# Kernel optimization log

Hardware: AMD Instinct MI355X
Metric: run time of the kernel (lower is better)

The kernel has to match this reference:

```python
import jax, jax.numpy as jnp
import numpy as np

NUM_NODES = 50000
NUM_EDGES = 800000
NUM_LABEL_EDGES = 100000
F_IN, F_HID, F_OUT = 128, 128, 64


def gcn_conv(x, src, dst, W, b, n):
    # PyG GCNConv: h = x @ W; add self-loops; symmetric normalization
    # deg counted on destination (col), including self-loop (+1).
    h = x @ W
    deg = jax.ops.segment_sum(jnp.ones(src.shape, h.dtype), dst, num_segments=n) + 1.0
    dinv = jax.lax.rsqrt(deg)  # deg >= 1 always (self-loop)
    norm = dinv[src] * dinv[dst]                       # [E]
    agg = jax.ops.segment_sum(h[src] * norm[:, None], dst, num_segments=n)
    agg = agg + h * (dinv * dinv)[:, None]             # self-loop term dinv[i]^2 * h[i]
    return agg + b


def setup_inputs() -> dict:
    key = jax.random.key(0)
    ks = jax.random.split(key, 9)
    x = jax.random.normal(ks[0], (NUM_NODES, F_IN), dtype=jnp.float32)
    edge_index = jax.random.randint(ks[1], (2, NUM_EDGES), 0, NUM_NODES, dtype=jnp.int64)
    edge_label_index = jax.random.randint(ks[2], (2, NUM_LABEL_EDGES), 0, NUM_NODES, dtype=jnp.int64)
    def glorot(k, fi, fo):
        s = (6.0 / (fi + fo)) ** 0.5
        return jax.random.uniform(k, (fi, fo), jnp.float32, -s, s)
    return {
        "x": x,
        "edge_index": edge_index,
        "edge_label_index": edge_label_index,
        "W1": glorot(ks[3], F_IN, F_HID),  "b1": jnp.zeros((F_HID,), jnp.float32),
        "W2": glorot(ks[4], F_HID, F_HID), "b2": jnp.zeros((F_HID,), jnp.float32),
        "W3": glorot(ks[5], F_HID, F_OUT), "b3": jnp.zeros((F_OUT,), jnp.float32),
    }


def reference(x, edge_index, edge_label_index, W1, b1, W2, b2, W3, b3):
    src, dst = edge_index[0], edge_index[1]
    z = jax.nn.relu(gcn_conv(x, src, dst, W1, b1, NUM_NODES))
    z = jax.nn.relu(gcn_conv(z, src, dst, W2, b2, NUM_NODES))
    z = gcn_conv(z, src, dst, W3, b3, NUM_NODES)
    # decode: dot product of endpoint embeddings per label edge
    return jnp.sum(z[edge_label_index[0]] * z[edge_label_index[1]], axis=-1)
```

## Files before the change

kernel.cpp:

```cpp
#include <hip/hip_runtime.h>
#include <hip/hip_bf16.h>
#include <stdint.h>

#define NN 50000
#define NE 800000
#define NL 100000
#define SLOTS 64
#define PADROW 50000

#define NB 196
#define BSH 8
#define BCAP 5376

typedef __attribute__((ext_vector_type(8))) short bf16x8;
typedef __attribute__((ext_vector_type(4))) float f32x4;
typedef __attribute__((ext_vector_type(4))) unsigned int u32x4;
typedef __attribute__((ext_vector_type(2))) unsigned int u32x2;
typedef __attribute__((ext_vector_type(8))) unsigned short u16x8;

__device__ __forceinline__ float asf(unsigned int u) {
    union { unsigned int i; float f; } c; c.i = u; return c.f;
}
__device__ __forceinline__ float bflo(unsigned int x) { return asf(x << 16); }
__device__ __forceinline__ float bfhi(unsigned int x) { return asf(x & 0xffff0000u); }
__device__ __forceinline__ unsigned short f2bf(float f) {
    union { float f; unsigned int i; } c; c.f = f;
    unsigned int u = c.i + (0x7fffu + ((c.i >> 16) & 1u));
    return (unsigned short)(u >> 16);
}

__device__ __forceinline__ void dma16(const unsigned short* g, char* l) {
    __builtin_amdgcn_global_load_lds(
        (const __attribute__((address_space(1))) unsigned int*)g,
        (__attribute__((address_space(3))) unsigned int*)l, 16, 0, 0);
}

__global__ void k_wprep(const float* __restrict__ W1, const float* __restrict__ W2,
                        const float* __restrict__ W3, unsigned short* __restrict__ Wt,
                        int* __restrict__ cursor, unsigned int* __restrict__ padA,
                        unsigned int* __restrict__ padB) {
    int idx = blockIdx.x * 256 + threadIdx.x;
    if (idx < NB) cursor[idx] = 0;
    if (idx < 64) padA[idx] = 0;
    else if (idx < 128) padB[idx - 64] = 0;
    const float* W; unsigned short* O; int base, Mloc;
    if (idx < 16384)      { W = W1; O = Wt;         base = idx;         Mloc = 128; }
    else if (idx < 32768) { W = W2; O = Wt + 16384; base = idx - 16384; Mloc = 128; }
    else                  { W = W3; O = Wt + 32768; base = idx - 32768; Mloc = 64;  }
    int n = base >> 7, k = base & 127;
    O[base] = f2bf(W[k * Mloc + n]);
}

__global__ __launch_bounds__(256) void k_bin(
        const int* __restrict__ src, const int* __restrict__ dst,
        int* __restrict__ cursor, unsigned int* __restrict__ binbuf) {
    __shared__ int hcnt[NB];
    __shared__ int hbase[NB];
    __shared__ unsigned int epk[2048];
    int tid = threadIdx.x;
    if (tid < NB) hcnt[tid] = 0;
    __syncthreads();
    int e0 = blockIdx.x * 2048;
    int e1 = min(e0 + 2048, NE);
    for (int e = e0 + tid; e < e1; e += 256) {
        int d = dst[e], s = src[e];
        atomicAdd(&hcnt[d >> BSH], 1);
        epk[e - e0] = (unsigned int)s | ((unsigned int)d << 16);
    }
    __syncthreads();
    if (tid < NB) { hbase[tid] = atomicAdd(&cursor[tid], hcnt[tid]); hcnt[tid] = 0; }
    __syncthreads();
    for (int e = e0 + tid; e < e1; e += 256) {
        unsigned int pk = epk[e - e0];
        int b = (int)(pk >> 16) >> BSH;
        int p = hbase[b] + atomicAdd(&hcnt[b], 1);
        if (p < BCAP)
            __builtin_nontemporal_store(pk, &binbuf[(size_t)b * BCAP + p]);
    }
}

__global__ __launch_bounds__(256) void k_csr(
        const unsigned int* __restrict__ binbuf, const int* __restrict__ cursor,
        int* __restrict__ deg, unsigned short* __restrict__ colp) {
    __shared__ unsigned short lcol[256 * SLOTS];
    __shared__ int ldeg[256];
    int tid = threadIdx.x;
    int blk = blockIdx.x;
    int base = blk << BSH;
    int nNodes = min(256, NN - base);
    ldeg[tid] = 0;
    const unsigned int fw = 0xC350C350u;
    u32x4 fill = {fw, fw, fw, fw};
    u32x4* lz = (u32x4*)lcol;
#pragma unroll
    for (int i = 0; i < 8; ++i) lz[i * 256 + tid] = fill;
    __syncthreads();
    int cnt = min(cursor[blk], BCAP);
    for (int e = tid; e < cnt; e += 256) {
        unsigned int pk = __builtin_nontemporal_load(&binbuf[(size_t)blk * BCAP + e]);
        int d = (int)(pk >> 16) - base;
        int p = atomicAdd(&ldeg[d], 1);
        if (p < SLOTS) {
            int pp = (p < 32) ? ((p & 3) * 8 + (p >> 2)) : p;
            lcol[d * SLOTS + pp] = (unsigned short)(pk & 0xffffu);
        }
    }
    __syncthreads();
    if (tid < nNodes) {
        int dv = ldeg[tid];
        deg[base + tid] = dv;
        if (dv < SLOTS) {
            int pp = (dv < 32) ? ((dv & 3) * 8 + (dv >> 2)) : dv;
            lcol[tid * SLOTS + pp] = (unsigned short)(base + tid);
        }
    }
    __syncthreads();
    u32x4* gout = (u32x4*)(colp + (size_t)base * SLOTS);
    const u32x4* lin = (const u32x4*)lcol;
    for (int i = tid; i < nNodes * 8; i += 256) gout[i] = lin[i];
}

__global__ __launch_bounds__(256) void k_gemm1(
        const float* __restrict__ A, const unsigned short* __restrict__ Wt,
        const int* __restrict__ deg, unsigned short* __restrict__ Outb, int N) {
    constexpr int K = 128;
    constexpr int NT = 8;
    int tid = threadIdx.x;
    int lane = tid & 63, wave = tid >> 6;
    int m = lane & 15, quad = lane >> 4;
    int rowA = blockIdx.x * 64 + wave * 16 + m;
    int rA = min(rowA, N - 1);

    bf16x8 afr[4];
    const float* p = A + (size_t)rA * K + quad * 8;
#pragma unroll
    for (int s = 0; s < 4; ++s) {
        float4 lo = *(const float4*)(p + s * 32);
        float4 hi = *(const float4*)(p + s * 32 + 4);
        bf16x8 r;
        r[0] = (short)f2bf(lo.x); r[1] = (short)f2bf(lo.y);
        r[2] = (short)f2bf(lo.z); r[3] = (short)f2bf(lo.w);
        r[4] = (short)f2bf(hi.x); r[5] = (short)f2bf(hi.y);
        r[6] = (short)f2bf(hi.z); r[7] = (short)f2bf(hi.w);
        afr[s] = r;
    }

    f32x4 acc[NT];
#pragma unroll
    for (int t = 0; t < NT; ++t) { acc[t][0] = 0.f; acc[t][1] = 0.f; acc[t][2] = 0.f; acc[t][3] = 0.f; }
#pragma unroll
    for (int t = 0; t < NT; ++t) {
        const unsigned short* wp = Wt + (size_t)(t * 16 + m) * K + quad * 8;
#pragma unroll
        for (int s = 0; s < 4; ++s) {
            bf16x8 bfr = *(const bf16x8*)(wp + s * 32);
            acc[t] = __builtin_amdgcn_mfma_f32_16x16x32_bf16(afr[s], bfr, acc[t], 0, 0, 0);
        }
    }

    int outRowBase = blockIdx.x * 64 + wave * 16 + quad * 4;
    float di[4];
#pragma unroll
    for (int i = 0; i < 4; ++i) di[i] = rsqrtf((float)deg[min(outRowBase + i, N - 1)] + 1.0f);
#pragma unroll
    for (int t = 0; t < NT; ++t)
#pragma unroll
        for (int i = 0; i < 4; ++i) {
            int rr = outRowBase + i;
            if (rr < N) Outb[(size_t)rr * 128 + t * 16 + m] = f2bf(acc[t][i] * di[i]);
        }
}

template <int M_>
__global__ __launch_bounds__(256) void k_agg_gemm(
        const unsigned short* __restrict__ hs, const int* __restrict__ deg,
        const unsigned short* __restrict__ colp, const float* __restrict__ bias,
        const unsigned short* __restrict__ Wt, unsigned short* __restrict__ Outb) {
    constexpr int K = 128;
    constexpr int NT = M_ / 64;
    __shared__ __align__(16) unsigned short As[16][136];
    __shared__ __align__(16) char stage[4][2][6144];
    int tid = threadIdx.x;
    int lane = tid & 63, wave = tid >> 6;
    int tileBase = blockIdx.x * 16;
    int g = lane >> 4, c = lane & 15;
    const unsigned short* hc = hs + c * 8;
    int nodeB = tileBase + wave * 4;

    int4 dg = *(const int4*)(deg + nodeB);
    int dgv[4] = {dg.x, dg.y, dg.z, dg.w};
    u16x8 sl4[4];
#pragma unroll
    for (int t = 0; t < 4; ++t)
        sl4[t] = *(const u16x8*)(colp + (unsigned)(nodeB + t) * SLOTS + g * 8);

    float bb[8];
    {
        const float4* bp = (const float4*)(bias + c * 8);
        float4 b0 = bp[0], b1 = bp[1];
        bb[0] = b0.x; bb[1] = b0.y; bb[2] = b0.z; bb[3] = b0.w;
        bb[4] = b1.x; bb[5] = b1.y; bb[6] = b1.z; bb[7] = b1.w;
    }

#pragma unroll
    for (int j = 0; j < 6; ++j)
        dma16(hc + (unsigned)sl4[0][j] * K, &stage[wave][0][j * 1024]);
#pragma unroll
    for (int j = 0; j < 6; ++j)
        dma16(hc + (unsigned)sl4[1][j] * K, &stage[wave][1][j * 1024]);

#pragma unroll
    for (int t = 0; t < 4; ++t) {
        int node = nodeB + t;
        int su = min(dgv[t] + 1, SLOTS);

        if (t < 3) asm volatile("s_waitcnt vmcnt(6)" ::: "memory");
        else       asm volatile("s_waitcnt vmcnt(0)" ::: "memory");
        __builtin_amdgcn_sched_barrier(0);

        const char* sb = &stage[wave][t & 1][0];
        float acc[8];
#pragma unroll
        for (int k = 0; k < 8; ++k) acc[k] = 0.f;
#pragma unroll
        for (int j = 0; j < 6; ++j) {
            u32x4 v = *(const u32x4*)(sb + j * 1024 + g * 256 + c * 16);
#pragma unroll
            for (int k = 0; k < 4; ++k) {
                acc[2 * k]     += bflo(v[k]);
                acc[2 * k + 1] += bfhi(v[k]);
            }
        }

        if (su > 24) {
            u32x4 w0 = *(const u32x4*)(hc + (unsigned)sl4[t][6] * K);
            u32x4 w1 = *(const u32x4*)(hc + (unsigned)sl4[t][7] * K);
#pragma unroll
            for (int k = 0; k < 4; ++k) {
                acc[2 * k]     += bflo(w0[k]) + bflo(w1[k]);
                acc[2 * k + 1] += bfhi(w0[k]) + bfhi(w1[k]);
            }
            if (su > 32) {
                u16x8 s2 = *(const u16x8*)(colp + (unsigned)node * SLOTS + 32 + g * 8);
#pragma unroll
                for (int h = 0; h < 8; ++h) {
                    u32x4 x = *(const u32x4*)(hc + (unsigned)s2[h] * K);
#pragma unroll
                    for (int k = 0; k < 4; ++k) {
                        acc[2 * k]     += bflo(x[k]);
                        acc[2 * k + 1] += bfhi(x[k]);
                    }
                }
            }
        }

        __builtin_amdgcn_sched_barrier(0);
        if (t < 2) {
#pragma unroll
            for (int j = 0; j < 6; ++j)
                dma16(hc + (unsigned)sl4[t + 2][j] * K,
                      &stage[wave][t & 1][j * 1024]);
        }

#pragma unroll
        for (int k = 0; k < 8; ++k) {
            acc[k] += __shfl_xor(acc[k], 16, 64);
            acc[k] += __shfl_xor(acc[k], 32, 64);
        }
        if (g == 0) {
            float di = rsqrtf((float)dgv[t] + 1.0f);
            u32x4 pv;
#pragma unroll
            for (int k = 0; k < 4; ++k) {
                float o0 = fmaxf(di * acc[2 * k]     + bb[2 * k],     0.f);
                float o1 = fmaxf(di * acc[2 * k + 1] + bb[2 * k + 1], 0.f);
                pv[k] = (unsigned int)f2bf(o0) | ((unsigned int)f2bf(o1) << 16);
            }
            *(u32x4*)&As[wave * 4 + t][c * 8] = pv;
        }
    }
    __syncthreads();

    int m = lane & 15, quad = lane >> 4;
    bf16x8 afr[4];
#pragma unroll
    for (int s = 0; s < 4; ++s)
        afr[s] = *(const bf16x8*)&As[m][s * 32 + quad * 8];

    f32x4 gacc[NT];
#pragma unroll
    for (int t = 0; t < NT; ++t) { gacc[t][0] = 0.f; gacc[t][1] = 0.f; gacc[t][2] = 0.f; gacc[t][3] = 0.f; }
#pragma unroll
    for (int t = 0; t < NT; ++t) {
        int ct = wave * NT + t;
        const unsigned short* wp = Wt + (size_t)(ct * 16 + m) * K + quad * 8;
#pragma unroll
        for (int s = 0; s < 4; ++s) {
            bf16x8 bfr = *(const bf16x8*)(wp + s * 32);
            gacc[t] = __builtin_amdgcn_mfma_f32_16x16x32_bf16(afr[s], bfr, gacc[t], 0, 0, 0);
        }
    }

    int rowBase = tileBase + quad * 4;
    int4 dg2 = *(const int4*)(deg + rowBase);
    int dgw[4] = {dg2.x, dg2.y, dg2.z, dg2.w};
    float di[4];
#pragma unroll
    for (int i = 0; i < 4; ++i) di[i] = rsqrtf((float)dgw[i] + 1.0f);
#pragma unroll
    for (int t = 0; t < NT; ++t) {
        int ct = wave * NT + t;
#pragma unroll
        for (int i = 0; i < 4; ++i)
            Outb[(size_t)(rowBase + i) * M_ + ct * 16 + m] = f2bf(gacc[t][i] * di[i]);
    }
}

__global__ __launch_bounds__(256, 8) void k_agg64(
        const unsigned short* __restrict__ hs, const int* __restrict__ deg,
        const unsigned short* __restrict__ colp, const float* __restrict__ bias,
        unsigned short* __restrict__ out, int n) {
    int tid = threadIdx.x;
    int wave = tid >> 6, lane = tid & 63;
    int node = blockIdx.x * 4 + wave;
    int g = lane >> 4, c = lane & 15;
    const unsigned short* hc = hs + c * 4;

    int degv = deg[node];
    int su = min(degv + 1, SLOTS);
    u16x8 sl = *(const u16x8*)(colp + (unsigned)node * SLOTS + g * 8);

    u32x2 vv[6];
#pragma unroll
    for (int k2 = 0; k2 < 6; ++k2)
        vv[k2] = *(const u32x2*)(hc + (unsigned)sl[k2] * 64);

    float acc[4] = {0.f, 0.f, 0.f, 0.f};
#pragma unroll
    for (int k2 = 0; k2 < 6; ++k2)
#pragma unroll
        for (int k = 0; k < 2; ++k) {
            acc[2 * k]     += bflo(vv[k2][k]);
            acc[2 * k + 1] += bfhi(vv[k2][k]);
        }
    if (su > 24) {
        u32x2 w0 = *(const u32x2*)(hc + (unsigned)sl[6] * 64);
        u32x2 w1 = *(const u32x2*)(hc + (unsigned)sl[7] * 64);
#pragma unroll
        for (int k = 0; k < 2; ++k) {
            acc[2 * k]     += bflo(w0[k]) + bflo(w1[k]);
            acc[2 * k + 1] += bfhi(w0[k]) + bfhi(w1[k]);
        }
        if (su > 32) {
            u16x8 s2 = *(const u16x8*)(colp + (unsigned)node * SLOTS + 32 + g * 8);
#pragma unroll
            for (int h = 0; h < 2; ++h) {
                u32x2 x0 = *(const u32x2*)(hc + (unsigned)s2[4 * h + 0] * 64);
                u32x2 x1 = *(const u32x2*)(hc + (unsigned)s2[4 * h + 1] * 64);
                u32x2 x2 = *(const u32x2*)(hc + (unsigned)s2[4 * h + 2] * 64);
                u32x2 x3 = *(const u32x2*)(hc + (unsigned)s2[4 * h + 3] * 64);
#pragma unroll
                for (int k = 0; k < 2; ++k) {
                    acc[2 * k]     += bflo(x0[k]) + bflo(x1[k]) + bflo(x2[k]) + bflo(x3[k]);
                    acc[2 * k + 1] += bfhi(x0[k]) + bfhi(x1[k]) + bfhi(x2[k]) + bfhi(x3[k]);
                }
            }
        }
    }
#pragma unroll
    for (int k = 0; k < 4; ++k) {
        acc[k] += __shfl_xor(acc[k], 16, 64);
        acc[k] += __shfl_xor(acc[k], 32, 64);
    }
    if (g == 0) {
        float di = rsqrtf((float)degv + 1.0f);
        float4 bb = *(const float4*)(bias + c * 4);
        u32x2 pv;
        pv[0] = (unsigned int)f2bf(di * acc[0] + bb.x) |
                ((unsigned int)f2bf(di * acc[1] + bb.y) << 16);
        pv[1] = (unsigned int)f2bf(di * acc[2] + bb.z) |
                ((unsigned int)f2bf(di * acc[3] + bb.w) << 16);
        *(u32x2*)(out + (size_t)node * 64 + c * 4) = pv;
    }
}

__global__ __launch_bounds__(256) void k_decode(
        const unsigned short* __restrict__ z, const int* __restrict__ ls,
        const int* __restrict__ ld, float* __restrict__ out, int nl) {
    int tid = threadIdx.x;
    int lane = tid & 63, wave = tid >> 6;
    int g = lane >> 3, c = lane & 7;
    int e = (blockIdx.x * 4 + wave) * 4 + (g >> 1);
    int row = (g & 1) ? ld[e] : ls[e];
    u32x4 v = *(const u32x4*)(z + (size_t)row * 64 + c * 8);
    u32x4 w;
#pragma unroll
    for (int k = 0; k < 4; ++k) w[k] = (unsigned int)__shfl_xor((int)v[k], 8, 64);
    float p = 0.f;
#pragma unroll
    for (int k = 0; k < 4; ++k)
        p += bflo(v[k]) * bflo(w[k]) + bfhi(v[k]) * bfhi(w[k]);
    p += __shfl_xor(p, 1, 64);
    p += __shfl_xor(p, 2, 64);
    p += __shfl_xor(p, 4, 64);
    if ((lane & 15) == 0) out[e] = p;
}


static inline size_t align256(size_t x) { return (x + 255) & ~(size_t)255; }

extern "C" void kernel_launch(void* const* d_in, const int* in_sizes, int n_in,
                              void* d_out, int out_size, void* d_ws, size_t ws_size,
                              hipStream_t stream) {
    const float* x  = (const float*)d_in[0];
    const int*   ei = (const int*)d_in[1];
    const int*   li = (const int*)d_in[2];
    const float* W1 = (const float*)d_in[3];
    const float* b1 = (const float*)d_in[4];
    const float* W2 = (const float*)d_in[5];
    const float* b2 = (const float*)d_in[6];
    const float* W3 = (const float*)d_in[7];
    const float* b3 = (const float*)d_in[8];
    float* out = (float*)d_out;

    const int* src = ei;
    const int* dst = ei + NE;
    const int* ls = li;
    const int* ld = li + NL;

    char* ws = (char*)d_ws;
    size_t off = 0;
    int* deg    = (int*)(ws + off); off += align256(NN * 4);
    int* cursor = (int*)(ws + off); off += align256(NB * 4);
    unsigned int* binbuf = (unsigned int*)(ws + off); off += align256((size_t)NB * BCAP * 4);
    unsigned short* colp = (unsigned short*)(ws + off); off += align256((size_t)NN * SLOTS * 2);
    unsigned short* Wtb  = (unsigned short*)(ws + off); off += align256(40960 * 2);
    unsigned short* bufA = (unsigned short*)(ws + off); off += align256(((size_t)NN * 128 + 128) * 2);
    unsigned short* bufB = (unsigned short*)(ws + off); off += align256(((size_t)NN * 128 + 128) * 2);
    unsigned short* bufZ = (unsigned short*)(ws + off); off += align256((size_t)NN * 64 * 2);
    unsigned short* h3 = bufA + (size_t)25000 * 128;

    k_wprep<<<160, 256, 0, stream>>>(W1, W2, W3, Wtb, cursor,
                                     (unsigned int*)(bufA + (size_t)PADROW * 128),
                                     (unsigned int*)(bufB + (size_t)PADROW * 128));
    k_bin<<<391, 256, 0, stream>>>(src, dst, cursor, binbuf);
    k_csr<<<NB, 256, 0, stream>>>(binbuf, cursor, deg, colp);

    k_gemm1<<<782, 256, 0, stream>>>(x, Wtb, deg, bufA, NN);
    k_agg_gemm<128><<<3125, 256, 0, stream>>>(bufA, deg, colp, b1, Wtb + 16384, bufB);
    k_agg_gemm<64><<<3125, 256, 0, stream>>>(bufB, deg, colp, b2, Wtb + 32768, h3);
    k_agg64<<<12500, 256, 0, stream>>>(h3, deg, colp, b3, bufZ, NN);
    k_decode<<<6250, 256, 0, stream>>>(bufZ, ls, ld, out, NL);
}
```

Measured before the change: 237.0 us.

## Pipeline final 64-wide aggregation via LDS DMA staging and shrink agg_gemm prefetch

Rewrites the final 64-feature aggregation kernel so each wave handles four nodes. It double-buffers neighbor-row gathers into LDS with async DMA and uses 16-byte lanes in an 8x8 layout, instead of one node per wave with direct 8-byte loads. In the fused aggregate+GEMM kernel, the LDS-prefetched slot groups per node drop from six to five, moving one group to the direct-load path. This reduces LDS footprint, which may raise occupancy. The costs are more LDS use in agg64, a deeper shuffle reduction, and more direct loads for mid-degree nodes.

New measurement: 246.2 us. 3.9% more time.

```diff
diff --git a/kernel.cpp b/kernel.cpp
--- a/kernel.cpp
+++ b/kernel.cpp
@@ -179,7 +179,7 @@
     constexpr int K = 128;
     constexpr int NT = M_ / 64;
     __shared__ __align__(16) unsigned short As[16][136];
-    __shared__ __align__(16) char stage[4][2][6144];
+    __shared__ __align__(16) char stage[4][2][5120];
     int tid = threadIdx.x;
     int lane = tid & 63, wave = tid >> 6;
     int tileBase = blockIdx.x * 16;
@@ -203,10 +203,10 @@
     }
 
 #pragma unroll
-    for (int j = 0; j < 6; ++j)
+    for (int j = 0; j < 5; ++j)
         dma16(hc + (unsigned)sl4[0][j] * K, &stage[wave][0][j * 1024]);
 #pragma unroll
-    for (int j = 0; j < 6; ++j)
+    for (int j = 0; j < 5; ++j)
         dma16(hc + (unsigned)sl4[1][j] * K, &stage[wave][1][j * 1024]);
 
 #pragma unroll
@@ -214,7 +214,7 @@
         int node = nodeB + t;
         int su = min(dgv[t] + 1, SLOTS);
 
-        if (t < 3) asm volatile("s_waitcnt vmcnt(6)" ::: "memory");
+        if (t < 3) asm volatile("s_waitcnt vmcnt(5)" ::: "memory");
         else       asm volatile("s_waitcnt vmcnt(0)" ::: "memory");
         __builtin_amdgcn_sched_barrier(0);
 
@@ -223,7 +223,7 @@
 #pragma unroll
         for (int k = 0; k < 8; ++k) acc[k] = 0.f;
 #pragma unroll
-        for (int j = 0; j < 6; ++j) {
+        for (int j = 0; j < 5; ++j) {
             u32x4 v = *(const u32x4*)(sb + j * 1024 + g * 256 + c * 16);
 #pragma unroll
             for (int k = 0; k < 4; ++k) {
@@ -232,13 +232,15 @@
             }
         }
 
-        if (su > 24) {
-            u32x4 w0 = *(const u32x4*)(hc + (unsigned)sl4[t][6] * K);
-            u32x4 w1 = *(const u32x4*)(hc + (unsigned)sl4[t][7] * K);
-#pragma unroll
-            for (int k = 0; k < 4; ++k) {
-                acc[2 * k]     += bflo(w0[k]) + bflo(w1[k]);
-                acc[2 * k + 1] += bfhi(w0[k]) + bfhi(w1[k]);
+        if (su > 20) {
+#pragma unroll
+            for (int j = 5; j < 8; ++j) {
+                u32x4 w = *(const u32x4*)(hc + (unsigned)sl4[t][j] * K);
+#pragma unroll
+                for (int k = 0; k < 4; ++k) {
+                    acc[2 * k]     += bflo(w[k]);
+                    acc[2 * k + 1] += bfhi(w[k]);
+                }
             }
             if (su > 32) {
                 u16x8 s2 = *(const u16x8*)(colp + (unsigned)node * SLOTS + 32 + g * 8);
@@ -257,7 +259,7 @@
         __builtin_amdgcn_sched_barrier(0);
         if (t < 2) {
 #pragma unroll
-            for (int j = 0; j < 6; ++j)
+            for (int j = 0; j < 5; ++j)
                 dma16(hc + (unsigned)sl4[t + 2][j] * K,
                       &stage[wave][t & 1][j * 1024]);
         }
@@ -316,71 +318,105 @@
     }
 }
 
-__global__ __launch_bounds__(256, 8) void k_agg64(
+__global__ __launch_bounds__(256) void k_agg64(
         const unsigned short* __restrict__ hs, const int* __restrict__ deg,
         const unsigned short* __restrict__ colp, const float* __restrict__ bias,
         unsigned short* __restrict__ out, int n) {
+    __shared__ __align__(16) char stage[4][2][4096];
     int tid = threadIdx.x;
     int wave = tid >> 6, lane = tid & 63;
-    int node = blockIdx.x * 4 + wave;
-    int g = lane >> 4, c = lane & 15;
-    const unsigned short* hc = hs + c * 4;
-
-    int degv = deg[node];
-    int su = min(degv + 1, SLOTS);
-    u16x8 sl = *(const u16x8*)(colp + (unsigned)node * SLOTS + g * 8);
-
-    u32x2 vv[6];
-#pragma unroll
-    for (int k2 = 0; k2 < 6; ++k2)
-        vv[k2] = *(const u32x2*)(hc + (unsigned)sl[k2] * 64);
-
-    float acc[4] = {0.f, 0.f, 0.f, 0.f};
-#pragma unroll
-    for (int k2 = 0; k2 < 6; ++k2)
-#pragma unroll
-        for (int k = 0; k < 2; ++k) {
-            acc[2 * k]     += bflo(vv[k2][k]);
-            acc[2 * k + 1] += bfhi(vv[k2][k]);
-        }
-    if (su > 24) {
-        u32x2 w0 = *(const u32x2*)(hc + (unsigned)sl[6] * 64);
-        u32x2 w1 = *(const u32x2*)(hc + (unsigned)sl[7] * 64);
-#pragma unroll
-        for (int k = 0; k < 2; ++k) {
-            acc[2 * k]     += bflo(w0[k]) + bflo(w1[k]);
-            acc[2 * k + 1] += bfhi(w0[k]) + bfhi(w1[k]);
-        }
+    int a = lane >> 3, c8 = lane & 7;
+    int nodeB = blockIdx.x * 16 + wave * 4;
+    const unsigned short* hc = hs + c8 * 8;
+
+    int4 dg = *(const int4*)(deg + nodeB);
+    int dgv[4] = {dg.x, dg.y, dg.z, dg.w};
+
+    unsigned short slv[4][4];
+#pragma unroll
+    for (int t = 0; t < 4; ++t)
+#pragma unroll
+        for (int j = 0; j < 4; ++j)
+            slv[t][j] = colp[(unsigned)(nodeB + t) * SLOTS + 8 * j + a];
+
+    float bb[8];
+    {
+        const float4* bp = (const float4*)(bias + c8 * 8);
+        float4 b0 = bp[0], b1 = bp[1];
+        bb[0] = b0.x; bb[1] = b0.y; bb[2] = b0.z; bb[3] = b0.w;
+        bb[4] = b1.x; bb[5] = b1.y; bb[6] = b1.z; bb[7] = b1.w;
+    }
+
+#pragma unroll
+    for (int j = 0; j < 4; ++j)
+        dma16(hc + (unsigned)slv[0][j] * 64, &stage[wave][0][j * 1024]);
+#pragma unroll
+    for (int j = 0; j < 4; ++j)
+        dma16(hc + (unsigned)slv[1][j] * 64, &stage[wave][1][j * 1024]);
+
+#pragma unroll
+    for (int t = 0; t < 4; ++t) {
+        int node = nodeB + t;
+        int su = min(dgv[t] + 1, SLOTS);
+
+        if (t < 3) asm volatile("s_waitcnt vmcnt(4)" ::: "memory");
+        else       asm volatile("s_waitcnt vmcnt(0)" ::: "memory");
+        __builtin_amdgcn_sched_barrier(0);
+
+        const char* sb = &stage[wave][t & 1][0];
+        float acc[8];
+#pragma unroll
+        for (int k = 0; k < 8; ++k) acc[k] = 0.f;
+#pragma unroll
+        for (int j = 0; j < 4; ++j) {
+            u32x4 v = *(const u32x4*)(sb + j * 1024 + a * 128 + c8 * 16);
+#pragma unroll
+            for (int k = 0; k < 4; ++k) {
+                acc[2 * k]     += bflo(v[k]);
+                acc[2 * k + 1] += bfhi(v[k]);
+            }
+        }
+
         if (su > 32) {
-            u16x8 s2 = *(const u16x8*)(colp + (unsigned)node * SLOTS + 32 + g * 8);
-#pragma unroll
-            for (int h = 0; h < 2; ++h) {
-                u32x2 x0 = *(const u32x2*)(hc + (unsigned)s2[4 * h + 0] * 64);
-                u32x2 x1 = *(const u32x2*)(hc + (unsigned)s2[4 * h + 1] * 64);
-                u32x2 x2 = *(const u32x2*)(hc + (unsigned)s2[4 * h + 2] * 64);
-                u32x2 x3 = *(const u32x2*)(hc + (unsigned)s2[4 * h + 3] * 64);
-#pragma unroll
-                for (int k = 0; k < 2; ++k) {
-                    acc[2 * k]     += bflo(x0[k]) + bflo(x1[k]) + bflo(x2[k]) + bflo(x3[k]);
-                    acc[2 * k + 1] += bfhi(x0[k]) + bfhi(x1[k]) + bfhi(x2[k]) + bfhi(x3[k]);
+            if (a < 4) {
+                u16x8 s2 = *(const u16x8*)(colp + (unsigned)node * SLOTS + 32 + a * 8);
+#pragma unroll
+                for (int h = 0; h < 8; ++h) {
+                    u32x4 x = *(const u32x4*)(hc + (unsigned)s2[h] * 64);
+#pragma unroll
+                    for (int k = 0; k < 4; ++k) {
+                        acc[2 * k]     += bflo(x[k]);
+                        acc[2 * k + 1] += bfhi(x[k]);
+                    }
                 }
             }
         }
-    }
-#pragma unroll
-    for (int k = 0; k < 4; ++k) {
-        acc[k] += __shfl_xor(acc[k], 16, 64);
-        acc[k] += __shfl_xor(acc[k], 32, 64);
-    }
-    if (g == 0) {
-        float di = rsqrtf((float)degv + 1.0f);
-        float4 bb = *(const float4*)(bias + c * 4);
-        u32x2 pv;
-        pv[0] = (unsigned int)f2bf(di * acc[0] + bb.x) |
-                ((unsigned int)f2bf(di * acc[1] + bb.y) << 16);
-        pv[1] = (unsigned int)f2bf(di * acc[2] + bb.z) |
-                ((unsigned int)f2bf(di * acc[3] + bb.w) << 16);
-        *(u32x2*)(out + (size_t)node * 64 + c * 4) = pv;
+
+        __builtin_amdgcn_sched_barrier(0);
+        if (t < 2) {
+#pragma unroll
+            for (int j = 0; j < 4; ++j)
+                dma16(hc + (unsigned)slv[t + 2][j] * 64,
+                      &stage[wave][t & 1][j * 1024]);
+        }
+
+#pragma unroll
+        for (int k = 0; k < 8; ++k) {
+            acc[k] += __shfl_xor(acc[k], 8, 64);
+            acc[k] += __shfl_xor(acc[k], 16, 64);
+            acc[k] += __shfl_xor(acc[k], 32, 64);
+        }
+        if (a == 0) {
+            float di = rsqrtf((float)dgv[t] + 1.0f);
+            u32x4 pv;
+#pragma unroll
+            for (int k = 0; k < 4; ++k) {
+                float o0 = di * acc[2 * k]     + bb[2 * k];
+                float o1 = di * acc[2 * k + 1] + bb[2 * k + 1];
+                pv[k] = (unsigned int)f2bf(o0) | ((unsigned int)f2bf(o1) << 16);
+            }
+            *(u32x4*)(out + (size_t)node * 64 + c8 * 8) = pv;
+        }
     }
 }
 
@@ -449,6 +485,6 @@
     k_gemm1<<<782, 256, 0, stream>>>(x, Wtb, deg, bufA, NN);
     k_agg_gemm<128><<<3125, 256, 0, stream>>>(bufA, deg, colp, b1, Wtb + 16384, bufB);
     k_agg_gemm<64><<<3125, 256, 0, stream>>>(bufB, deg, colp, b2, Wtb + 32768, h3);
-    k_agg64<<<12500, 256, 0, stream>>>(h3, deg, colp, b3, bufZ, NN);
+    k_agg64<<<3125, 256, 0, stream>>>(h3, deg, colp, b3, bufZ, NN);
     k_decode<<<6250, 256, 0, stream>>>(bufZ, ls, ld, out, NL);
 }
```
